# Performance work log

Measured on AMD Instinct MI355X. Metric: run time of the kernel, lower is better.

Reference implementation:

```python
import jax, jax.numpy as jnp
import numpy as np

N = 50000      # nodes
E = 800000     # edges (before self-loops)
IN_C = 128
HID = 32
HEADS = 4
OUT_C = 64
NEG_SLOPE = 0.2


def setup_inputs() -> dict:
    key = jax.random.key(0)
    ks = jax.random.split(key, 10)
    x = jax.random.normal(ks[0], (N, IN_C), dtype=jnp.float32)
    edge_index = jax.random.randint(ks[1], (2, E), 0, N, dtype=jnp.int32)
    # layer 1 params (GATConv(in_c, hid_c, heads=4), concat=True)
    W1 = jax.random.normal(ks[2], (IN_C, HEADS * HID), dtype=jnp.float32) / np.sqrt(IN_C)
    a_src1 = jax.random.normal(ks[3], (HEADS, HID), dtype=jnp.float32) / np.sqrt(HID)
    a_dst1 = jax.random.normal(ks[4], (HEADS, HID), dtype=jnp.float32) / np.sqrt(HID)
    b1 = jnp.zeros((HEADS * HID,), dtype=jnp.float32)
    # layer 2 params (GATConv(hid_c*heads, out_c, heads=1))
    W2 = jax.random.normal(ks[5], (HEADS * HID, OUT_C), dtype=jnp.float32) / np.sqrt(HEADS * HID)
    a_src2 = jax.random.normal(ks[6], (1, OUT_C), dtype=jnp.float32) / np.sqrt(OUT_C)
    a_dst2 = jax.random.normal(ks[7], (1, OUT_C), dtype=jnp.float32) / np.sqrt(OUT_C)
    b2 = jnp.zeros((OUT_C,), dtype=jnp.float32)
    return {"x": x, "edge_index": edge_index, "W1": W1, "a_src1": a_src1,
            "a_dst1": a_dst1, "b1": b1, "W2": W2, "a_src2": a_src2,
            "a_dst2": a_dst2, "b2": b2}


def _gat_layer(x, src, dst, self_mask, W, a_s, a_d, b, n):
    """One PyG-style GATConv: concat heads, leaky_relu(0.2), scatter-softmax over dst."""
    H, F = a_s.shape
    h = (x @ W).reshape(n, H, F)                       # [N, H, F]
    al_s = jnp.einsum('nhf,hf->nh', h, a_s)            # [N, H]
    al_d = jnp.einsum('nhf,hf->nh', h, a_d)
    e = al_s[src] + al_d[dst]                          # [E', H]
    e = jnp.where(e >= 0, e, NEG_SLOPE * e)            # leaky relu
    # emulate remove_self_loops on original edges (appended loops not masked)
    e = jnp.where(self_mask[:, None], -1e30, e)
    m = jax.ops.segment_max(e, dst, num_segments=n)    # per-dst max for stability
    p = jnp.exp(e - m[dst])
    p = jnp.where(self_mask[:, None], 0.0, p)
    denom = jax.ops.segment_sum(p, dst, num_segments=n) + 1e-16
    alpha = p / denom[dst]                             # [E', H]
    out = jax.ops.segment_sum(alpha[:, :, None] * h[src], dst, num_segments=n)
    return out.reshape(n, H * F) + b


def reference(x, edge_index, W1, a_src1, a_dst1, b1, W2, a_src2, a_dst2, b2):
    n = x.shape[0]
    src, dst = edge_index[0], edge_index[1]
    loops = jnp.arange(n, dtype=edge_index.dtype)
    src_a = jnp.concatenate([src, loops])
    dst_a = jnp.concatenate([dst, loops])
    # mask pre-existing self-loops (PyG removes then re-adds self loops)
    self_mask = jnp.concatenate([src == dst, jnp.zeros((n,), dtype=bool)])
    h = _gat_layer(x, src_a, dst_a, self_mask, W1, a_src1, a_dst1, b1, n)
    h = jax.nn.relu(h)
    return _gat_layer(h, src_a, dst_a, self_mask, W2, a_src2, a_dst2, b2, n)
```

## Files before the change

### kernel.cpp

```cpp
#include <hip/hip_runtime.h>

typedef unsigned short u16;
typedef unsigned int u32;
typedef __attribute__((ext_vector_type(8))) short bf16x8;
typedef __attribute__((ext_vector_type(4))) float f32x4;

__device__ __forceinline__ float bf(u16 u){ return __uint_as_float(((u32)u) << 16); }
__device__ __forceinline__ float bf_lo(u32 u){ return __uint_as_float(u << 16); }
__device__ __forceinline__ float bf_hi(u32 u){ return __uint_as_float(u & 0xFFFF0000u); }
__device__ __forceinline__ u16 to_bf16(float f){
    u32 x = __float_as_uint(f);
    u32 r = (x + 0x7FFFu + ((x >> 16) & 1u)) >> 16;
    return (u16)r;
}
__device__ __forceinline__ float leaky(float v){ return (v >= 0.f) ? v : 0.2f * v; }
__device__ __forceinline__ float eexp(float v){
    return __expf(fminf(leaky(v), 80.f));
}
__device__ __forceinline__ float ldany(const void* p, int i, int fl){
    return fl ? bf(((const u16*)p)[i]) : ((const float*)p)[i];
}
__device__ __forceinline__ u16 ldany_bf(const void* p, int i, int fl){
    return fl ? ((const u16*)p)[i] : to_bf16(((const float*)p)[i]);
}

constexpr int NS = 256;

struct HistCvtArgs {
    const int* dst; const int* src; int E; int chE; u16* cnt; int NBIN;
    const void* xin; u16* Xb; int nx;
    const void* W1; const void* W2; u16* W1t; u16* W2t;
    const void* vin[6]; float* vout[6];
    int* flag;
};
__global__ __launch_bounds__(256) void hist_cvt(HistCvtArgs a){
    int b = blockIdx.x;
    if (b < NS){
        __shared__ u32 hist[128];
        if (threadIdx.x < 128) hist[threadIdx.x] = 0;
        __syncthreads();
        int s0 = b * a.chE, s1 = min(a.E, s0 + a.chE);
        for (int i = s0 + threadIdx.x; i < s1; i += 256){
            int d = a.dst[i];
            if (a.src[i] != d) atomicAdd(&hist[d >> 9], 1);
        }
        __syncthreads();
        if (threadIdx.x < a.NBIN)
            a.cnt[threadIdx.x * NS + b] = (u16)hist[threadIdx.x];
        return;
    }
    __shared__ int sflag;
    const u16* x16 = (const u16*)a.xin;
    if (threadIdx.x < 64){
        int ok = 1;
        for (int i = threadIdx.x; i < 256; i += 64){
            u16 v = x16[i];
            int e = (v >> 7) & 0xFF;
            if (!((e >= 100 && e <= 140) || (v & 0x7FFFu) == 0)) ok = 0;
        }
        unsigned long long bl = __ballot(ok);
        if (threadIdx.x == 0) sflag = (__popcll(bl) >= 62) ? 1 : 0;
    }
    __syncthreads();
    int fl = sflag;
    int ci = (b - NS) * 256 + threadIdx.x;
    if (ci == 0) *a.flag = fl;
    if (ci < a.nx){ a.Xb[ci] = ldany_bf(a.xin, ci, fl); return; }
    ci -= a.nx;
    if (ci < 128 * 128){
        int n = ci >> 7, k = ci & 127;
        a.W1t[ci] = ldany_bf(a.W1, k * 128 + n, fl);
        return;
    }
    ci -= 128 * 128;
    if (ci < 64 * 128){
        int n = ci >> 7, k = ci & 127;
        a.W2t[ci] = ldany_bf(a.W2, k * 64 + n, fl);
        return;
    }
    ci -= 64 * 128;
    const int vsz[6] = {128, 128, 128, 64, 64, 64};
    #pragma unroll
    for (int s = 0; s < 6; s++){
        if (ci < vsz[s]){ a.vout[s][ci] = ldany(a.vin[s], ci, fl); return; }
        ci -= vsz[s];
    }
}

__global__ __launch_bounds__(1024) void scan_cnt(const u16* __restrict__ cnt,
                                                 u32* __restrict__ S, int NBIN){
    __shared__ int wsum[16];
    int t = threadIdx.x;
    int M = NBIN * NS;
    int C = (M + 1023) / 1024;
    int f0 = t * C;
    u32 c[32];
    int s = 0;
    #pragma unroll
    for (int i = 0; i < 32; i++){
        int f = f0 + i;
        u32 v = (i < C && f < M) ? (u32)cnt[f] : 0u;
        c[i] = v;
        s += (int)v;
    }
    int v = s;
    #pragma unroll
    for (int d = 1; d < 64; d <<= 1){
        int o = __shfl_up(v, d);
        if ((t & 63) >= d) v += o;
    }
    if ((t & 63) == 63) wsum[t >> 6] = v;
    __syncthreads();
    int woff = 0;
    for (int wv = 0; wv < (t >> 6); wv++) woff += wsum[wv];
    int run = woff + v - s;
    #pragma unroll
    for (int i = 0; i < 32; i++){
        int f = f0 + i;
        if (i < C && f < M){
            S[f] = run;
            run += (int)c[i];
        }
    }
    if (t == 1023) S[M] = run;
}

struct BucketGemmArgs {
    const int* dst; const int* src; int E; int chE; const u32* S; int NBIN;
    u32* bucket;
    const u16* Xb; const u16* W1t; u16* HB;
    const float* a_s; const float* a_d; float* al_s; float* al_d;
    int N;
};
__global__ __launch_bounds__(256) void bucket_gemm(BucketGemmArgs a){
    int b = blockIdx.x;
    if (b < NS){
        __shared__ u32 cur[128];
        if (threadIdx.x < a.NBIN) cur[threadIdx.x] = a.S[threadIdx.x * NS + b];
        __syncthreads();
        int s0 = b * a.chE, s1 = min(a.E, s0 + a.chE);
        for (int i = s0 + threadIdx.x; i < s1; i += 256){
            int d = a.dst[i];
            int s = a.src[i];
            if (s != d){
                u32 pos = atomicAdd(&cur[d >> 9], 1);
                a.bucket[pos] = ((u32)d << 16) | (u32)s;
            }
        }
        return;
    }
    int gb = b - NS;
    int lane = threadIdx.x & 63;
    int w = threadIdx.x >> 6;
    int row0 = gb * 64 + w * 16;
    int m = lane & 15, quad = lane >> 4;
    int arow = row0 + m;
    if (arow >= a.N) arow = a.N - 1;
    f32x4 acc[8];
    #pragma unroll
    for (int j = 0; j < 8; j++) acc[j] = (f32x4){0.f, 0.f, 0.f, 0.f};
    const u16* ap = a.Xb + (size_t)arow * 128 + quad * 8;
    const u16* bp = a.W1t + (size_t)m * 128 + quad * 8;
    #pragma unroll
    for (int kc = 0; kc < 4; kc++){
        bf16x8 av = *(const bf16x8*)(ap + kc * 32);
        #pragma unroll
        for (int nb = 0; nb < 8; nb++){
            bf16x8 bv = *(const bf16x8*)(bp + nb * 16 * 128 + kc * 32);
            acc[nb] = __builtin_amdgcn_mfma_f32_16x16x32_bf16(av, bv, acc[nb], 0, 0, 0);
        }
    }
    #pragma unroll
    for (int nb = 0; nb < 8; nb++){
        #pragma unroll
        for (int r = 0; r < 4; r++){
            int grow = row0 + quad * 4 + r;
            if (grow < a.N) a.HB[(size_t)grow * 128 + nb * 16 + m] = to_bf16(acc[nb][r]);
        }
    }
    float asr[8], adr[8];
    #pragma unroll
    for (int nb = 0; nb < 8; nb++){ asr[nb] = a.a_s[nb * 16 + m]; adr[nb] = a.a_d[nb * 16 + m]; }
    #pragma unroll
    for (int r = 0; r < 4; r++){
        int grow = row0 + quad * 4 + r;
        #pragma unroll
        for (int h = 0; h < 4; h++){
            float ps = acc[2 * h][r] * asr[2 * h] + acc[2 * h + 1][r] * asr[2 * h + 1];
            float pd = acc[2 * h][r] * adr[2 * h] + acc[2 * h + 1][r] * adr[2 * h + 1];
            #pragma unroll
            for (int d = 1; d < 16; d <<= 1){
                ps += __shfl_xor(ps, d);
                pd += __shfl_xor(pd, d);
            }
            if (m == h && grow < a.N){
                a.al_s[grow * 4 + h] = ps;
                a.al_d[grow * 4 + h] = pd;
            }
        }
    }
}

__global__ __launch_bounds__(256) void bin_csr(const u32* __restrict__ S,
                                               const u32* __restrict__ bucket,
                                               int* __restrict__ off,
                                               u16* __restrict__ csr,
                                               int N, int NBIN){
    __shared__ u32 degL[512];
    __shared__ u32 curL[512];
    __shared__ int wsum[4];
    int b = blockIdx.x, t = threadIdx.x;
    int lo = b << 9;
    u32 base = S[b * NS];
    u32 end  = S[(b + 1) * NS];
    degL[t] = 0; degL[t + 256] = 0;
    __syncthreads();
    for (u32 i = base + t; i < end; i += 256){
        u32 pr = bucket[i];
        atomicAdd(&degL[(pr >> 16) - lo], 1);
    }
    __syncthreads();
    u32 d0 = degL[2 * t], d1 = degL[2 * t + 1];
    int p = (int)(d0 + d1);
    int v = p;
    #pragma unroll
    for (int d = 1; d < 64; d <<= 1){
        int o = __shfl_up(v, d);
        if ((t & 63) >= d) v += o;
    }
    if ((t & 63) == 63) wsum[t >> 6] = v;
    __syncthreads();
    int woff = 0;
    for (int wv = 0; wv < (t >> 6); wv++) woff += wsum[wv];
    int eb = woff + v - p;
    curL[2 * t] = eb;
    curL[2 * t + 1] = eb + d0;
    int n0 = lo + 2 * t, n1 = lo + 2 * t + 1;
    if (n0 < N) off[n0] = (int)(base + eb);
    if (n1 < N) off[n1] = (int)(base + eb + d0);
    if (b == NBIN - 1 && t == 255) off[N] = (int)end;
    __syncthreads();
    for (u32 i = base + t; i < end; i += 256){
        u32 pr = bucket[i];
        u32 pos = base + atomicAdd(&curL[(pr >> 16) - lo], 1);
        csr[pos] = (u16)(pr & 0xFFFF);
    }
}

__global__ __launch_bounds__(256) void gemm2_logits(const u16* __restrict__ Xb,
                                                    const u16* __restrict__ Wt,
                                                    u16* __restrict__ HB,
                                                    const float* __restrict__ a_s,
                                                    const float* __restrict__ a_d,
                                                    float* __restrict__ al_s,
                                                    float* __restrict__ al_d, int N){
    int lane = threadIdx.x & 63;
    int w = threadIdx.x >> 6;
    int row0 = blockIdx.x * 64 + w * 16;
    int m = lane & 15, quad = lane >> 4;
    int arow = row0 + m;
    if (arow >= N) arow = N - 1;
    f32x4 acc[4];
    #pragma unroll
    for (int j = 0; j < 4; j++) acc[j] = (f32x4){0.f, 0.f, 0.f, 0.f};
    const u16* ap = Xb + (size_t)arow * 128 + quad * 8;
    const u16* bp = Wt + (size_t)m * 128 + quad * 8;
    #pragma unroll
    for (int kc = 0; kc < 4; kc++){
        bf16x8 av = *(const bf16x8*)(ap + kc * 32);
        #pragma unroll
        for (int nb = 0; nb < 4; nb++){
            bf16x8 bv = *(const bf16x8*)(bp + nb * 16 * 128 + kc * 32);
            acc[nb] = __builtin_amdgcn_mfma_f32_16x16x32_bf16(av, bv, acc[nb], 0, 0, 0);
        }
    }
    #pragma unroll
    for (int nb = 0; nb < 4; nb++){
        #pragma unroll
        for (int r = 0; r < 4; r++){
            int grow = row0 + quad * 4 + r;
            if (grow < N) HB[(size_t)grow * 64 + nb * 16 + m] = to_bf16(acc[nb][r]);
        }
    }
    float asr[4], adr[4];
    #pragma unroll
    for (int nb = 0; nb < 4; nb++){ asr[nb] = a_s[nb * 16 + m]; adr[nb] = a_d[nb * 16 + m]; }
    #pragma unroll
    for (int r = 0; r < 4; r++){
        int grow = row0 + quad * 4 + r;
        float ps = 0.f, pd = 0.f;
        #pragma unroll
        for (int nb = 0; nb < 4; nb++){ ps += acc[nb][r] * asr[nb]; pd += acc[nb][r] * adr[nb]; }
        #pragma unroll
        for (int d = 1; d < 16; d <<= 1){
            ps += __shfl_xor(ps, d);
            pd += __shfl_xor(pd, d);
        }
        if (m == 0 && grow < N){
            al_s[grow] = ps;
            al_d[grow] = pd;
        }
    }
}

__global__ __launch_bounds__(256) void gat_agg1(const int* __restrict__ off,
                                                const u16* __restrict__ csr,
                                                const u16* __restrict__ h1,
                                                const float* __restrict__ als,
                                                const float* __restrict__ ald,
                                                const float* __restrict__ b1,
                                                u16* __restrict__ outm, int N){
    int lane = threadIdx.x & 63;
    int n = blockIdx.x * 4 + (threadIdx.x >> 6);
    if (n >= N) return;
    int o0 = off[n], o1 = off[n + 1];
    int q = lane >> 4, ql = lane & 15;
    int c0 = ql * 8;
    int head = ql >> 2;
    float aldh = ald[n * 4 + head];
    float acc[8] = {};
    float s = 0.f;
    int j = o0 + q;
    for (; j + 4 < o1; j += 8){
        int sc0 = csr[j], sc1 = csr[j + 4];
        float e0 = eexp(als[sc0 * 4 + head] + aldh);
        float e1 = eexp(als[sc1 * 4 + head] + aldh);
        uint4 u0 = *(const uint4*)&h1[(size_t)sc0 * 128 + c0];
        uint4 u1 = *(const uint4*)&h1[(size_t)sc1 * 128 + c0];
        s += e0 + e1;
        acc[0] += e0 * bf_lo(u0.x) + e1 * bf_lo(u1.x);
        acc[1] += e0 * bf_hi(u0.x) + e1 * bf_hi(u1.x);
        acc[2] += e0 * bf_lo(u0.y) + e1 * bf_lo(u1.y);
        acc[3] += e0 * bf_hi(u0.y) + e1 * bf_hi(u1.y);
        acc[4] += e0 * bf_lo(u0.z) + e1 * bf_lo(u1.z);
        acc[5] += e0 * bf_hi(u0.z) + e1 * bf_hi(u1.z);
        acc[6] += e0 * bf_lo(u0.w) + e1 * bf_lo(u1.w);
        acc[7] += e0 * bf_hi(u0.w) + e1 * bf_hi(u1.w);
    }
    if (j < o1){
        int sc = csr[j];
        float e = eexp(als[sc * 4 + head] + aldh);
        uint4 u = *(const uint4*)&h1[(size_t)sc * 128 + c0];
        s += e;
        acc[0] += e * bf_lo(u.x); acc[1] += e * bf_hi(u.x);
        acc[2] += e * bf_lo(u.y); acc[3] += e * bf_hi(u.y);
        acc[4] += e * bf_lo(u.z); acc[5] += e * bf_hi(u.z);
        acc[6] += e * bf_lo(u.w); acc[7] += e * bf_hi(u.w);
    }
    s += __shfl_xor(s, 16);
    s += __shfl_xor(s, 32);
    #pragma unroll
    for (int i = 0; i < 8; i++){
        acc[i] += __shfl_xor(acc[i], 16);
        acc[i] += __shfl_xor(acc[i], 32);
    }
    if (q == 0){
        float esx = eexp(als[n * 4 + head] + aldh);
        float inv = 1.f / (s + esx + 1e-16f);
        uint4 u = *(const uint4*)&h1[(size_t)n * 128 + c0];
        acc[0] += esx * bf_lo(u.x); acc[1] += esx * bf_hi(u.x);
        acc[2] += esx * bf_lo(u.y); acc[3] += esx * bf_hi(u.y);
        acc[4] += esx * bf_lo(u.z); acc[5] += esx * bf_hi(u.z);
        acc[6] += esx * bf_lo(u.w); acc[7] += esx * bf_hi(u.w);
        float4 bA = *(const float4*)&b1[c0];
        float4 bB = *(const float4*)&b1[c0 + 4];
        u16 pk[8];
        pk[0] = to_bf16(fmaxf(acc[0] * inv + bA.x, 0.f));
        pk[1] = to_bf16(fmaxf(acc[1] * inv + bA.y, 0.f));
        pk[2] = to_bf16(fmaxf(acc[2] * inv + bA.z, 0.f));
        pk[3] = to_bf16(fmaxf(acc[3] * inv + bA.w, 0.f));
        pk[4] = to_bf16(fmaxf(acc[4] * inv + bB.x, 0.f));
        pk[5] = to_bf16(fmaxf(acc[5] * inv + bB.y, 0.f));
        pk[6] = to_bf16(fmaxf(acc[6] * inv + bB.z, 0.f));
        pk[7] = to_bf16(fmaxf(acc[7] * inv + bB.w, 0.f));
        *(uint4*)&outm[(size_t)n * 128 + c0] = *(uint4*)pk;
    }
}

__global__ __launch_bounds__(256) void gat_agg2(const int* __restrict__ off,
                                                const u16* __restrict__ csr,
                                                const u16* __restrict__ h2,
                                                const float* __restrict__ als,
                                                const float* __restrict__ ald,
                                                const float* __restrict__ b2,
                                                void* __restrict__ outv, int N,
                                                const int* __restrict__ flag){
    int lane = threadIdx.x & 63;
    int n = blockIdx.x * 4 + (threadIdx.x >> 6);
    if (n >= N) return;
    int o0 = off[n], o1 = off[n + 1];
    int oc = lane >> 3, ol = lane & 7;
    int c0 = ol * 8;
    float aldn = ald[n];
    float acc[8] = {};
    float s = 0.f;
    int j = o0 + oc;
    for (; j + 8 < o1; j += 16){
        int sc0 = csr[j], sc1 = csr[j + 8];
        float e0 = eexp(als[sc0] + aldn);
        float e1 = eexp(als[sc1] + aldn);
        uint4 u0 = *(const uint4*)&h2[(size_t)sc0 * 64 + c0];
        uint4 u1 = *(const uint4*)&h2[(size_t)sc1 * 64 + c0];
        s += e0 + e1;
        acc[0] += e0 * bf_lo(u0.x) + e1 * bf_lo(u1.x);
        acc[1] += e0 * bf_hi(u0.x) + e1 * bf_hi(u1.x);
        acc[2] += e0 * bf_lo(u0.y) + e1 * bf_lo(u1.y);
        acc[3] += e0 * bf_hi(u0.y) + e1 * bf_hi(u1.y);
        acc[4] += e0 * bf_lo(u0.z) + e1 * bf_lo(u1.z);
        acc[5] += e0 * bf_hi(u0.z) + e1 * bf_hi(u1.z);
        acc[6] += e0 * bf_lo(u0.w) + e1 * bf_lo(u1.w);
        acc[7] += e0 * bf_hi(u0.w) + e1 * bf_hi(u1.w);
    }
    if (j < o1){
        int sc = csr[j];
        float e = eexp(als[sc] + aldn);
        uint4 u = *(const uint4*)&h2[(size_t)sc * 64 + c0];
        s += e;
        acc[0] += e * bf_lo(u.x); acc[1] += e * bf_hi(u.x);
        acc[2] += e * bf_lo(u.y); acc[3] += e * bf_hi(u.y);
        acc[4] += e * bf_lo(u.z); acc[5] += e * bf_hi(u.z);
        acc[6] += e * bf_lo(u.w); acc[7] += e * bf_hi(u.w);
    }
    s += __shfl_xor(s, 8);
    s += __shfl_xor(s, 16);
    s += __shfl_xor(s, 32);
    #pragma unroll
    for (int i = 0; i < 8; i++){
        acc[i] += __shfl_xor(acc[i], 8);
        acc[i] += __shfl_xor(acc[i], 16);
        acc[i] += __shfl_xor(acc[i], 32);
    }
    if (oc == 0){
        float esx = eexp(als[n] + aldn);
        float inv = 1.f / (s + esx + 1e-16f);
        uint4 u = *(const uint4*)&h2[(size_t)n * 64 + c0];
        acc[0] += esx * bf_lo(u.x); acc[1] += esx * bf_hi(u.x);
        acc[2] += esx * bf_lo(u.y); acc[3] += esx * bf_hi(u.y);
        acc[4] += esx * bf_lo(u.z); acc[5] += esx * bf_hi(u.z);
        acc[6] += esx * bf_lo(u.w); acc[7] += esx * bf_hi(u.w);
        float4 bA = *(const float4*)&b2[c0];
        float4 bB = *(const float4*)&b2[c0 + 4];
        float r[8];
        r[0] = acc[0] * inv + bA.x; r[1] = acc[1] * inv + bA.y;
        r[2] = acc[2] * inv + bA.z; r[3] = acc[3] * inv + bA.w;
        r[4] = acc[4] * inv + bB.x; r[5] = acc[5] * inv + bB.y;
        r[6] = acc[6] * inv + bB.z; r[7] = acc[7] * inv + bB.w;
        if (*flag){
            u16 pk[8];
            #pragma unroll
            for (int i = 0; i < 8; i++) pk[i] = to_bf16(r[i]);
            *(uint4*)&((u16*)outv)[(size_t)n * 64 + c0] = *(uint4*)pk;
        } else {
            float* op = &((float*)outv)[(size_t)n * 64 + c0];
            *(float4*)op = make_float4(r[0], r[1], r[2], r[3]);
            *(float4*)(op + 4) = make_float4(r[4], r[5], r[6], r[7]);
        }
    }
}

extern "C" void kernel_launch(void* const* d_in, const int* in_sizes, int n_in,
                              void* d_out, int out_size, void* d_ws, size_t ws_size,
                              hipStream_t stream){
    const int* ei  = (const int*)d_in[1];
    const int N = in_sizes[0] / 128;
    const int E = in_sizes[1] / 2;
    const int* src = ei;
    const int* dst = ei + E;
    const int NBIN = (N + 511) >> 9;
    const int chE  = (E + NS - 1) / NS;

    char* w = (char*)d_ws;
    auto alloc = [&](size_t bytes){ char* p = w; w += (bytes + 255) & ~(size_t)255; return p; };
    int*   flag  = (int*)  alloc(4);
    u16*   cnt   = (u16*)  alloc((size_t)NS * NBIN * 2);
    u32*   S     = (u32*)  alloc(((size_t)NS * NBIN + 1) * 4);
    u32*   bucket= (u32*)  alloc((size_t)E * 4);
    int*   off   = (int*)  alloc((size_t)(N + 1) * 4);
    u16*   csr   = (u16*)  alloc((size_t)E * 2);
    u16*   W1t   = (u16*)  alloc(128 * 128 * 2);
    u16*   W2t   = (u16*)  alloc(64 * 128 * 2);
    float* as1f  = (float*)alloc(128 * 4);
    float* ad1f  = (float*)alloc(128 * 4);
    float* b1f   = (float*)alloc(128 * 4);
    float* as2f  = (float*)alloc(64 * 4);
    float* ad2f  = (float*)alloc(64 * 4);
    float* b2f   = (float*)alloc(64 * 4);
    u16*   Xb    = (u16*)  alloc((size_t)N * 128 * 2);
    u16*   h1b   = (u16*)  alloc((size_t)N * 128 * 2);
    u16*   hmidb = (u16*)  alloc((size_t)N * 128 * 2);
    u16*   h2b   = (u16*)  alloc((size_t)N * 64 * 2);
    float* als1  = (float*)alloc((size_t)N * 4 * 4);
    float* ald1  = (float*)alloc((size_t)N * 4 * 4);
    float* als2  = als1;
    float* ald2  = ald1;

    HistCvtArgs k1;
    k1.dst = dst; k1.src = src; k1.E = E; k1.chE = chE; k1.cnt = cnt; k1.NBIN = NBIN;
    k1.xin = d_in[0]; k1.Xb = Xb; k1.nx = N * 128;
    k1.W1 = d_in[2]; k1.W2 = d_in[6]; k1.W1t = W1t; k1.W2t = W2t;
    const void* vin[6]  = {d_in[3], d_in[4], d_in[5], d_in[7], d_in[8], d_in[9]};
    float* vout[6] = {as1f, ad1f, b1f, as2f, ad2f, b2f};
    for (int s = 0; s < 6; s++){ k1.vin[s] = vin[s]; k1.vout[s] = vout[s]; }
    k1.flag = flag;
    int cvt_total = N * 128 + 128 * 128 + 64 * 128 + 576;
    hist_cvt<<<NS + (cvt_total + 255) / 256, 256, 0, stream>>>(k1);

    scan_cnt<<<1, 1024, 0, stream>>>(cnt, S, NBIN);

    BucketGemmArgs k3;
    k3.dst = dst; k3.src = src; k3.E = E; k3.chE = chE; k3.S = S; k3.NBIN = NBIN;
    k3.bucket = bucket;
    k3.Xb = Xb; k3.W1t = W1t; k3.HB = h1b;
    k3.a_s = as1f; k3.a_d = ad1f; k3.al_s = als1; k3.al_d = ald1;
    k3.N = N;
    bucket_gemm<<<NS + (N + 63) / 64, 256, 0, stream>>>(k3);

    bin_csr<<<NBIN, 256, 0, stream>>>(S, bucket, off, csr, N, NBIN);

    gat_agg1<<<(N + 3) / 4, 256, 0, stream>>>(off, csr, h1b, als1, ald1, b1f, hmidb, N);

    gemm2_logits<<<(N + 63) / 64, 256, 0, stream>>>(hmidb, W2t, h2b, as2f, ad2f, als2, ald2, N);

    gat_agg2<<<(N + 3) / 4, 256, 0, stream>>>(off, csr, h2b, als2, ald2, b2f, d_out, N, flag);
}
```

Measured before the change: 245.1 us.

## Fold count scan into bucket kernel and unroll aggregation with packed math

Removes the single-block scan_cnt launch. Each bucketing block now recomputes its own per-bin prefix offsets directly from the count matrix, and block 0 writes the per-bin totals that bin_csr needs. This drops one serialized launch and its dependency, at the cost of redundant per-block reads of the count rows. The layer-1 aggregation loop is also unrolled to four neighbours per iteration, and both aggregation kernels use float2 vector accumulators so the compiler can emit packed FMAs.

```diff
diff --git a/kernel.cpp b/kernel.cpp
--- a/kernel.cpp
+++ b/kernel.cpp
@@ -4,6 +4,7 @@
 typedef unsigned int u32;
 typedef __attribute__((ext_vector_type(8))) short bf16x8;
 typedef __attribute__((ext_vector_type(4))) float f32x4;
+typedef __attribute__((ext_vector_type(2))) float f32x2;
 
 __device__ __forceinline__ float bf(u16 u){ return __uint_as_float(((u32)u) << 16); }
 __device__ __forceinline__ float bf_lo(u32 u){ return __uint_as_float(u << 16); }
@@ -16,6 +17,9 @@
 __device__ __forceinline__ float leaky(float v){ return (v >= 0.f) ? v : 0.2f * v; }
 __device__ __forceinline__ float eexp(float v){
     return __expf(fminf(leaky(v), 80.f));
+}
+__device__ __forceinline__ f32x2 unpk2(u32 u){
+    return (f32x2){bf_lo(u), bf_hi(u)};
 }
 __device__ __forceinline__ float ldany(const void* p, int i, int fl){
     return fl ? bf(((const u16*)p)[i]) : ((const float*)p)[i];
@@ -87,46 +91,9 @@
     }
 }
 
-__global__ __launch_bounds__(1024) void scan_cnt(const u16* __restrict__ cnt,
-                                                 u32* __restrict__ S, int NBIN){
-    __shared__ int wsum[16];
-    int t = threadIdx.x;
-    int M = NBIN * NS;
-    int C = (M + 1023) / 1024;
-    int f0 = t * C;
-    u32 c[32];
-    int s = 0;
-    #pragma unroll
-    for (int i = 0; i < 32; i++){
-        int f = f0 + i;
-        u32 v = (i < C && f < M) ? (u32)cnt[f] : 0u;
-        c[i] = v;
-        s += (int)v;
-    }
-    int v = s;
-    #pragma unroll
-    for (int d = 1; d < 64; d <<= 1){
-        int o = __shfl_up(v, d);
-        if ((t & 63) >= d) v += o;
-    }
-    if ((t & 63) == 63) wsum[t >> 6] = v;
-    __syncthreads();
-    int woff = 0;
-    for (int wv = 0; wv < (t >> 6); wv++) woff += wsum[wv];
-    int run = woff + v - s;
-    #pragma unroll
-    for (int i = 0; i < 32; i++){
-        int f = f0 + i;
-        if (i < C && f < M){
-            S[f] = run;
-            run += (int)c[i];
-        }
-    }
-    if (t == 1023) S[M] = run;
-}
-
 struct BucketGemmArgs {
-    const int* dst; const int* src; int E; int chE; const u32* S; int NBIN;
+    const int* dst; const int* src; int E; int chE; const u16* cnt; int NBIN;
+    u32* Sbin;
     u32* bucket;
     const u16* Xb; const u16* W1t; u16* HB;
     const float* a_s; const float* a_d; float* al_s; float* al_d;
@@ -136,10 +103,31 @@
     int b = blockIdx.x;
     if (b < NS){
         __shared__ u32 cur[128];
-        if (threadIdx.x < a.NBIN) cur[threadIdx.x] = a.S[threadIdx.x * NS + b];
+        __shared__ u32 Tl[129];
+        int t = threadIdx.x;
+        if (t < a.NBIN){
+            const u16* row = a.cnt + (size_t)t * NS;
+            u32 cb = 0, tot = 0;
+            for (int sx = 0; sx < NS; sx++){
+                u32 v = row[sx];
+                tot += v;
+                cb += (sx < b) ? v : 0u;
+            }
+            Tl[t + 1] = tot;
+            cur[t] = cb;
+        }
+        __syncthreads();
+        if (t == 0){
+            u32 run = 0;
+            Tl[0] = 0;
+            for (int g = 1; g <= a.NBIN; g++){ run += Tl[g]; Tl[g] = run; }
+        }
+        __syncthreads();
+        if (t < a.NBIN) cur[t] += Tl[t];
+        if (b == 0 && t <= a.NBIN) a.Sbin[t] = Tl[t];
         __syncthreads();
         int s0 = b * a.chE, s1 = min(a.E, s0 + a.chE);
-        for (int i = s0 + threadIdx.x; i < s1; i += 256){
+        for (int i = s0 + t; i < s1; i += 256){
             int d = a.dst[i];
             int s = a.src[i];
             if (s != d){
@@ -201,7 +189,7 @@
     }
 }
 
-__global__ __launch_bounds__(256) void bin_csr(const u32* __restrict__ S,
+__global__ __launch_bounds__(256) void bin_csr(const u32* __restrict__ Sbin,
                                                const u32* __restrict__ bucket,
                                                int* __restrict__ off,
                                                u16* __restrict__ csr,
@@ -211,8 +199,8 @@
     __shared__ int wsum[4];
     int b = blockIdx.x, t = threadIdx.x;
     int lo = b << 9;
-    u32 base = S[b * NS];
-    u32 end  = S[(b + 1) * NS];
+    u32 base = Sbin[b];
+    u32 end  = Sbin[b + 1];
     degL[t] = 0; degL[t + 256] = 0;
     __syncthreads();
     for (u32 i = base + t; i < end; i += 256){
@@ -318,35 +306,40 @@
     int c0 = ql * 8;
     int head = ql >> 2;
     float aldh = ald[n * 4 + head];
-    float acc[8] = {};
+    f32x2 a0 = {0.f, 0.f}, a1 = {0.f, 0.f}, a2 = {0.f, 0.f}, a3 = {0.f, 0.f};
     float s = 0.f;
     int j = o0 + q;
-    for (; j + 4 < o1; j += 8){
-        int sc0 = csr[j], sc1 = csr[j + 4];
+    for (; j + 12 < o1; j += 16){
+        int sc0 = csr[j], sc1 = csr[j + 4], sc2 = csr[j + 8], sc3 = csr[j + 12];
         float e0 = eexp(als[sc0 * 4 + head] + aldh);
         float e1 = eexp(als[sc1 * 4 + head] + aldh);
+        float e2 = eexp(als[sc2 * 4 + head] + aldh);
+        float e3 = eexp(als[sc3 * 4 + head] + aldh);
         uint4 u0 = *(const uint4*)&h1[(size_t)sc0 * 128 + c0];
         uint4 u1 = *(const uint4*)&h1[(size_t)sc1 * 128 + c0];
-        s += e0 + e1;
-        acc[0] += e0 * bf_lo(u0.x) + e1 * bf_lo(u1.x);
-        acc[1] += e0 * bf_hi(u0.x) + e1 * bf_hi(u1.x);
-        acc[2] += e0 * bf_lo(u0.y) + e1 * bf_lo(u1.y);
-        acc[3] += e0 * bf_hi(u0.y) + e1 * bf_hi(u1.y);
-        acc[4] += e0 * bf_lo(u0.z) + e1 * bf_lo(u1.z);
-        acc[5] += e0 * bf_hi(u0.z) + e1 * bf_hi(u1.z);
-        acc[6] += e0 * bf_lo(u0.w) + e1 * bf_lo(u1.w);
-        acc[7] += e0 * bf_hi(u0.w) + e1 * bf_hi(u1.w);
-    }
-    if (j < o1){
+        uint4 u2 = *(const uint4*)&h1[(size_t)sc2 * 128 + c0];
+        uint4 u3 = *(const uint4*)&h1[(size_t)sc3 * 128 + c0];
+        s += (e0 + e1) + (e2 + e3);
+        f32x2 ev0 = {e0, e0}, ev1 = {e1, e1}, ev2 = {e2, e2}, ev3 = {e3, e3};
+        a0 += ev0 * unpk2(u0.x); a1 += ev0 * unpk2(u0.y);
+        a2 += ev0 * unpk2(u0.z); a3 += ev0 * unpk2(u0.w);
+        a0 += ev1 * unpk2(u1.x); a1 += ev1 * unpk2(u1.y);
+        a2 += ev1 * unpk2(u1.z); a3 += ev1 * unpk2(u1.w);
+        a0 += ev2 * unpk2(u2.x); a1 += ev2 * unpk2(u2.y);
+        a2 += ev2 * unpk2(u2.z); a3 += ev2 * unpk2(u2.w);
+        a0 += ev3 * unpk2(u3.x); a1 += ev3 * unpk2(u3.y);
+        a2 += ev3 * unpk2(u3.z); a3 += ev3 * unpk2(u3.w);
+    }
+    for (; j < o1; j += 4){
         int sc = csr[j];
         float e = eexp(als[sc * 4 + head] + aldh);
         uint4 u = *(const uint4*)&h1[(size_t)sc * 128 + c0];
         s += e;
-        acc[0] += e * bf_lo(u.x); acc[1] += e * bf_hi(u.x);
-        acc[2] += e * bf_lo(u.y); acc[3] += e * bf_hi(u.y);
-        acc[4] += e * bf_lo(u.z); acc[5] += e * bf_hi(u.z);
-        acc[6] += e * bf_lo(u.w); acc[7] += e * bf_hi(u.w);
-    }
+        f32x2 ev = {e, e};
+        a0 += ev * unpk2(u.x); a1 += ev * unpk2(u.y);
+        a2 += ev * unpk2(u.z); a3 += ev * unpk2(u.w);
+    }
+    float acc[8] = {a0.x, a0.y, a1.x, a1.y, a2.x, a2.y, a3.x, a3.y};
     s += __shfl_xor(s, 16);
     s += __shfl_xor(s, 32);
     #pragma unroll
@@ -392,7 +385,7 @@
     int oc = lane >> 3, ol = lane & 7;
     int c0 = ol * 8;
     float aldn = ald[n];
-    float acc[8] = {};
+    f32x2 a0 = {0.f, 0.f}, a1 = {0.f, 0.f}, a2 = {0.f, 0.f}, a3 = {0.f, 0.f};
     float s = 0.f;
     int j = o0 + oc;
     for (; j + 8 < o1; j += 16){
@@ -402,25 +395,22 @@
         uint4 u0 = *(const uint4*)&h2[(size_t)sc0 * 64 + c0];
         uint4 u1 = *(const uint4*)&h2[(size_t)sc1 * 64 + c0];
         s += e0 + e1;
-        acc[0] += e0 * bf_lo(u0.x) + e1 * bf_lo(u1.x);
-        acc[1] += e0 * bf_hi(u0.x) + e1 * bf_hi(u1.x);
-        acc[2] += e0 * bf_lo(u0.y) + e1 * bf_lo(u1.y);
-        acc[3] += e0 * bf_hi(u0.y) + e1 * bf_hi(u1.y);
-        acc[4] += e0 * bf_lo(u0.z) + e1 * bf_lo(u1.z);
-        acc[5] += e0 * bf_hi(u0.z) + e1 * bf_hi(u1.z);
-        acc[6] += e0 * bf_lo(u0.w) + e1 * bf_lo(u1.w);
-        acc[7] += e0 * bf_hi(u0.w) + e1 * bf_hi(u1.w);
+        f32x2 ev0 = {e0, e0}, ev1 = {e1, e1};
+        a0 += ev0 * unpk2(u0.x); a1 += ev0 * unpk2(u0.y);
+        a2 += ev0 * unpk2(u0.z); a3 += ev0 * unpk2(u0.w);
+        a0 += ev1 * unpk2(u1.x); a1 += ev1 * unpk2(u1.y);
+        a2 += ev1 * unpk2(u1.z); a3 += ev1 * unpk2(u1.w);
     }
     if (j < o1){
         int sc = csr[j];
         float e = eexp(als[sc] + aldn);
         uint4 u = *(const uint4*)&h2[(size_t)sc * 64 + c0];
         s += e;
-        acc[0] += e * bf_lo(u.x); acc[1] += e * bf_hi(u.x);
-        acc[2] += e * bf_lo(u.y); acc[3] += e * bf_hi(u.y);
-        acc[4] += e * bf_lo(u.z); acc[5] += e * bf_hi(u.z);
-        acc[6] += e * bf_lo(u.w); acc[7] += e * bf_hi(u.w);
-    }
+        f32x2 ev = {e, e};
+        a0 += ev * unpk2(u.x); a1 += ev * unpk2(u.y);
+        a2 += ev * unpk2(u.z); a3 += ev * unpk2(u.w);
+    }
+    float acc[8] = {a0.x, a0.y, a1.x, a1.y, a2.x, a2.y, a3.x, a3.y};
     s += __shfl_xor(s, 8);
     s += __shfl_xor(s, 16);
     s += __shfl_xor(s, 32);
@@ -473,7 +463,7 @@
     auto alloc = [&](size_t bytes){ char* p = w; w += (bytes + 255) & ~(size_t)255; return p; };
     int*   flag  = (int*)  alloc(4);
     u16*   cnt   = (u16*)  alloc((size_t)NS * NBIN * 2);
-    u32*   S     = (u32*)  alloc(((size_t)NS * NBIN + 1) * 4);
+    u32*   Sbin  = (u32*)  alloc((size_t)(NBIN + 1) * 4);
     u32*   bucket= (u32*)  alloc((size_t)E * 4);
     int*   off   = (int*)  alloc((size_t)(N + 1) * 4);
     u16*   csr   = (u16*)  alloc((size_t)E * 2);
@@ -505,17 +495,16 @@
     int cvt_total = N * 128 + 128 * 128 + 64 * 128 + 576;
     hist_cvt<<<NS + (cvt_total + 255) / 256, 256, 0, stream>>>(k1);
 
-    scan_cnt<<<1, 1024, 0, stream>>>(cnt, S, NBIN);
-
     BucketGemmArgs k3;
-    k3.dst = dst; k3.src = src; k3.E = E; k3.chE = chE; k3.S = S; k3.NBIN = NBIN;
+    k3.dst = dst; k3.src = src; k3.E = E; k3.chE = chE; k3.cnt = cnt; k3.NBIN = NBIN;
+    k3.Sbin = Sbin;
     k3.bucket = bucket;
     k3.Xb = Xb; k3.W1t = W1t; k3.HB = h1b;
     k3.a_s = as1f; k3.a_d = ad1f; k3.al_s = als1; k3.al_d = ald1;
     k3.N = N;
     bucket_gemm<<<NS + (N + 63) / 64, 256, 0, stream>>>(k3);
 
-    bin_csr<<<NBIN, 256, 0, stream>>>(S, bucket, off, csr, N, NBIN);
+    bin_csr<<<NBIN, 256, 0, stream>>>(Sbin, bucket, off, csr, N, NBIN);
 
     gat_agg1<<<(N + 3) / 4, 256, 0, stream>>>(off, csr, h1b, als1, ald1, b1f, hmidb, N);
 
```

Result: faster. 229.5 us (median of 2 runs) (-6.4%).
